# Optimization experiments

Measured on AMD Instinct MI355X. Metric: run time of the kernel, lower is better.

Reference implementation:

```python
import jax, jax.numpy as jnp
import numpy as np

# Shapes hard-coded by the original module
B, C1, C2, S, K, H, E = 128, 128, 14, 14, 3, 256, 2  # batch, chan-split, chan-split, spatial, kernel, hidden, expand


def setup_inputs() -> dict:
    key = jax.random.key(0)
    k1, k2, k3 = jax.random.split(key, 3)
    x = jax.random.normal(k1, (B, C1 * C2, S), dtype=jnp.float32)
    w0 = jax.random.normal(k2, (H, E), dtype=jnp.float32)        # weights[0]
    w1 = jax.random.normal(k3, (C1, K, H), dtype=jnp.float32)    # weights[1]
    return {"x": x, "w0": w0, "w1": w1, "shift": 1}


def reference(x, w0, w1, shift):
    # reshape to (B, C1, C2, S); original torch treats it as (B, 1792, 14, 1)
    xr = x.reshape(B, C1, C2, S)
    # unfold((3,1), padding=(1,0)): 1D im2col along the S (=14) axis
    xp = jnp.pad(xr, ((0, 0), (0, 0), (0, 0), (1, 1)))
    # patches[b, j, n, i, m] = xp[b, j, n, m + i]  -> (B, C1, C2, K, S)
    patches = jnp.stack([xp[..., k:k + S] for k in range(K)], axis=3)
    # einsum 'ljnmi,jik->lnmk' (torch had m,i swapped via permute; fold it in)
    t4 = jnp.einsum('ljnim,jik->lnmk', patches, w1)   # (B, C2, S, H)
    # einsum 'kmlj,ji->kmlji': outer product with w0 along a new expand dim
    t5 = t4[..., None] * w0                            # (B, C2, S, H, E)
    t5 = jnp.roll(t5, shift, axis=1)                   # cyclic shift over C2
    t6 = jnp.transpose(t5, (0, 2, 3, 1, 4)).reshape(B, S, H, C2 * E)
    t6 = jnp.roll(t6, shift, axis=3)                   # cyclic shift over merged (C2*E)
    t6 = t6.reshape(B, S, H, C2, E).sum(axis=4)        # (B, S, H, C2)
    return jnp.transpose(t6, (0, 2, 3, 1))             # (B, H, C2, S) = (128, 256, 14, 14)
```

## Files before the change

kernel.cpp:

```cpp
#include <hip/hip_runtime.h>
#include <hip/hip_bf16.h>
#include <math.h>

#define B_   128
#define C1_  128
#define C2_  14
#define S_   14
#define K_   3
#define H_   256
#define E_   2

#define HT   64
#define NT   4
#define MT   13
#define CH   64
#define XSTR 72
#define BSTR 200
#define CSTR 68

typedef __attribute__((ext_vector_type(8))) short bf16x8;
typedef __attribute__((ext_vector_type(4))) float f32x4;

__device__ __forceinline__ unsigned short f2bf(float f) {
    unsigned int u = __float_as_uint(f);
    return (unsigned short)((u + 0x7FFF + ((u >> 16) & 1)) >> 16);
}

__device__ __forceinline__ int decode_shift(const int* p) {
    int a = p[0];
    if (a >= -100 && a <= 100 && a != 0) return a;
    float f = __int_as_float(a);
    if (f >= -100.f && f <= 100.f && f == truncf(f) && f != 0.f) return (int)f;
    long long bits = ((long long)p[1] << 32) | (unsigned int)a;
    double d = __longlong_as_double(bits);
    if (d >= -100.0 && d <= 100.0 && d == trunc(d) && d != 0.0) return (int)d;
    return a;
}

__global__ __launch_bounds__(256, 2) void fused_kernel(const float* __restrict__ x,
                                                       const float* __restrict__ w0,
                                                       const float* __restrict__ w1,
                                                       const int* __restrict__ shift_p,
                                                       float* __restrict__ out) {
    __shared__ __align__(16) char lds[60160];
    unsigned short* xT = (unsigned short*)lds;
    unsigned short* Bt = (unsigned short*)(lds + 34560);
    float*          Cl = (float*)lds;

    const int b    = blockIdx.x >> 2;
    const int h0   = (blockIdx.x & 3) * HT;
    const int t    = threadIdx.x;
    const int wave = t >> 6;
    const int lane = t & 63;
    const int quad = lane >> 4;
    const int l15  = lane & 15;

    f32x4 acc[4][NT];
#pragma unroll
    for (int i = 0; i < 4; ++i)
#pragma unroll
        for (int j = 0; j < NT; ++j) acc[i][j] = (f32x4){0.f, 0.f, 0.f, 0.f};

    for (int hf = 0; hf < 2; ++hf) {
        if (hf) __syncthreads();
        const float* xb = x + ((size_t)b * C1_ + hf * CH) * (C2_ * S_);
        for (int idx = t; idx < CH * 196; idx += 256) {
            int c1l = idx / 196, cs = idx - c1l * 196;
            int c2 = cs / S_, s = cs - c2 * S_;
            xT[(c2 * 16 + s + 1) * XSTR + c1l] = f2bf(xb[c1l * 196 + cs]);
        }
        for (int idx = t; idx < C2_ * CH * 2; idx += 256) {
            int c2 = idx / (CH * 2), r = idx - c2 * CH * 2;
            int p = (r < CH) ? 0 : 15, c1l = (r < CH) ? r : r - CH;
            xT[(c2 * 16 + p) * XSTR + c1l] = 0;
        }
        for (int idx = t; idx < CH * K_ * HT; idx += 256) {
            int hl = idx & (HT - 1);
            int rest = idx >> 6;
            int kk = rest / CH, c1l = rest - kk * CH;
            Bt[hl * BSTR + kk * CH + c1l] =
                f2bf(w1[((size_t)(hf * CH + c1l) * K_ + kk) * H_ + h0 + hl]);
        }
        __syncthreads();

#pragma unroll
        for (int tt = 0; tt < 6; ++tt) {
            const int kk = tt >> 1;
            const int c1off = (tt & 1) * 32 + quad * 8;
            bf16x8 bf[NT];
#pragma unroll
            for (int nc = 0; nc < NT; ++nc)
                bf[nc] = *(const bf16x8*)&Bt[(nc * 16 + l15) * BSTR + tt * 32 + quad * 8];
#pragma unroll
            for (int mi = 0; mi < 4; ++mi) {
                int mt = wave + mi * 4;
                if (mt < MT) {
                    int r = mt * 16 + l15;
                    int c2 = r / 14, s = r - c2 * 14;
                    bf16x8 af = *(const bf16x8*)&xT[(c2 * 16 + s + kk) * XSTR + c1off];
#pragma unroll
                    for (int nc = 0; nc < NT; ++nc)
                        acc[mi][nc] = __builtin_amdgcn_mfma_f32_16x16x32_bf16(
                            af, bf[nc], acc[mi][nc], 0, 0, 0);
                }
            }
        }
    }

    __syncthreads();
#pragma unroll
    for (int mi = 0; mi < 4; ++mi) {
        int mt = wave + mi * 4;
        if (mt < MT) {
#pragma unroll
            for (int nc = 0; nc < NT; ++nc) {
                int hl = nc * 16 + l15;
#pragma unroll
                for (int reg = 0; reg < 4; ++reg)
                    Cl[(mt * 16 + quad * 4 + reg) * CSTR + hl] = acc[mi][nc][reg];
            }
        }
    }
    __syncthreads();

    const int shift = decode_shift(shift_p);
    for (int idx = t; idx < HT * 196; idx += 256) {
        int hl = idx / 196, nm = idx - hl * 196;
        int n = nm / S_, m = nm - n * S_;
        int h = h0 + hl;
        float v = 0.f;
#pragma unroll
        for (int e = 0; e < E_; ++e) {
            int q = (2 * n + e - shift) % (C2_ * E_); if (q < 0) q += C2_ * E_;
            int np = q >> 1, ep = q & 1;
            int c2 = (np - shift) % C2_; if (c2 < 0) c2 += C2_;
            v += w0[h * E_ + ep] * Cl[(c2 * S_ + m) * CSTR + hl];
        }
        out[((size_t)(b * H_ + h) * C2_ + n) * S_ + m] = v;
    }
}

extern "C" void kernel_launch(void* const* d_in, const int* in_sizes, int n_in,
                              void* d_out, int out_size, void* d_ws, size_t ws_size,
                              hipStream_t stream) {
    const float* x     = (const float*)d_in[0];
    const float* w0    = (const float*)d_in[1];
    const float* w1    = (const float*)d_in[2];
    const int*   shift = (const int*)(n_in > 3 ? d_in[3] : d_in[n_in - 1]);
    for (int i = 0; i < n_in; ++i) {
        int sz = in_sizes[i];
        if (sz == B_ * C1_ * C2_ * S_)      x     = (const float*)d_in[i];
        else if (sz == H_ * E_)             w0    = (const float*)d_in[i];
        else if (sz == C1_ * K_ * H_)       w1    = (const float*)d_in[i];
        else if (sz == 1)                   shift = (const int*)d_in[i];
    }
    float* out = (float*)d_out;

    fused_kernel<<<B_ * (H_ / HT), 256, 0, stream>>>(x, w0, w1, shift, out);
}
```

Measured before the change: 109.2 us.

## Pre-convert inputs to bf16 in a separate kernel and vectorize LDS staging/epilogue

Adds a conversion kernel that writes x and w1 as bf16 into workspace, so the fused kernel reads half the bytes and does not convert each element redundantly across the four h-blocks per batch. LDS fills are restructured so each thread gathers 8 channels and writes one 16-byte vector. The C tile is stored transposed (h-major) with vector stores, and the epilogue hoists the shift index math per row. The cost is an extra kernel launch plus a full extra read and write pass over x through workspace memory.

```diff
diff --git a/kernel.cpp b/kernel.cpp
--- a/kernel.cpp
+++ b/kernel.cpp
@@ -16,14 +16,16 @@
 #define CH   64
 #define XSTR 72
 #define BSTR 200
-#define CSTR 68
-
+#define CROW 212
+
+typedef unsigned short u16;
+typedef unsigned int   u32;
 typedef __attribute__((ext_vector_type(8))) short bf16x8;
 typedef __attribute__((ext_vector_type(4))) float f32x4;
 
-__device__ __forceinline__ unsigned short f2bf(float f) {
-    unsigned int u = __float_as_uint(f);
-    return (unsigned short)((u + 0x7FFF + ((u >> 16) & 1)) >> 16);
+__device__ __forceinline__ u16 f2bf(float f) {
+    u32 u = __float_as_uint(f);
+    return (u16)((u + 0x7FFF + ((u >> 16) & 1)) >> 16);
 }
 
 __device__ __forceinline__ int decode_shift(const int* p) {
@@ -37,15 +39,32 @@
     return a;
 }
 
-__global__ __launch_bounds__(256, 2) void fused_kernel(const float* __restrict__ x,
+__global__ __launch_bounds__(256) void cvt_kernel(const float* __restrict__ x,
+                                                  const float* __restrict__ w1,
+                                                  u16* __restrict__ xb,
+                                                  u16* __restrict__ w1b) {
+    const int NXq = (B_ * C1_ * C2_ * S_) / 4;
+    const int NWq = (C1_ * K_ * H_) / 4;
+    int q = blockIdx.x * 256 + threadIdx.x;
+    float4 v; u16* dst;
+    if (q < NXq)      { v = ((const float4*)x)[q];        dst = xb  + (size_t)q * 4; }
+    else { int r = q - NXq; if (r >= NWq) return;
+                       v = ((const float4*)w1)[r];        dst = w1b + (size_t)r * 4; }
+    u32 lo = (u32)f2bf(v.x) | ((u32)f2bf(v.y) << 16);
+    u32 hi = (u32)f2bf(v.z) | ((u32)f2bf(v.w) << 16);
+    *(uint2*)dst = make_uint2(lo, hi);
+}
+
+template <bool PRE>
+__global__ __launch_bounds__(256, 2) void fused_kernel(const void* __restrict__ xsrc,
                                                        const float* __restrict__ w0,
-                                                       const float* __restrict__ w1,
+                                                       const void* __restrict__ wsrc,
                                                        const int* __restrict__ shift_p,
                                                        float* __restrict__ out) {
     __shared__ __align__(16) char lds[60160];
-    unsigned short* xT = (unsigned short*)lds;
-    unsigned short* Bt = (unsigned short*)(lds + 34560);
-    float*          Cl = (float*)lds;
+    u16*   xT = (u16*)lds;
+    u16*   Bt = (u16*)(lds + 34560);
+    float* Cl = (float*)lds;
 
     const int b    = blockIdx.x >> 2;
     const int h0   = (blockIdx.x & 3) * HT;
@@ -63,23 +82,59 @@
 
     for (int hf = 0; hf < 2; ++hf) {
         if (hf) __syncthreads();
-        const float* xb = x + ((size_t)b * C1_ + hf * CH) * (C2_ * S_);
-        for (int idx = t; idx < CH * 196; idx += 256) {
-            int c1l = idx / 196, cs = idx - c1l * 196;
-            int c2 = cs / S_, s = cs - c2 * S_;
-            xT[(c2 * 16 + s + 1) * XSTR + c1l] = f2bf(xb[c1l * 196 + cs]);
-        }
-        for (int idx = t; idx < C2_ * CH * 2; idx += 256) {
-            int c2 = idx / (CH * 2), r = idx - c2 * CH * 2;
-            int p = (r < CH) ? 0 : 15, c1l = (r < CH) ? r : r - CH;
-            xT[(c2 * 16 + p) * XSTR + c1l] = 0;
-        }
-        for (int idx = t; idx < CH * K_ * HT; idx += 256) {
-            int hl = idx & (HT - 1);
-            int rest = idx >> 6;
-            int kk = rest / CH, c1l = rest - kk * CH;
-            Bt[hl * BSTR + kk * CH + c1l] =
-                f2bf(w1[((size_t)(hf * CH + c1l) * K_ + kk) * H_ + h0 + hl]);
+        {
+            const int oct = t >> 5, cs0 = t & 31;
+            const int c1b = hf * CH + oct * 8;
+#pragma unroll
+            for (int i = 0; i < 7; ++i) {
+                int cs = cs0 + 32 * i;
+                if (cs < 196) {
+                    int c2 = cs / 14, s = cs - c2 * 14;
+                    u16 v[8];
+                    if (PRE) {
+                        const u16* xbp = (const u16*)xsrc + (size_t)b * (C1_ * 196);
+#pragma unroll
+                        for (int j = 0; j < 8; ++j) v[j] = xbp[(c1b + j) * 196 + cs];
+                    } else {
+                        const float* xf = (const float*)xsrc + (size_t)b * (C1_ * 196);
+#pragma unroll
+                        for (int j = 0; j < 8; ++j) v[j] = f2bf(xf[(c1b + j) * 196 + cs]);
+                    }
+                    u32 w[4];
+#pragma unroll
+                    for (int j = 0; j < 4; ++j) w[j] = (u32)v[2 * j] | ((u32)v[2 * j + 1] << 16);
+                    *(uint4*)&xT[(c2 * 16 + s + 1) * XSTR + oct * 8] = make_uint4(w[0], w[1], w[2], w[3]);
+                }
+            }
+            if (t < 224) {
+                int c2 = t >> 4, r = t & 15;
+                int p = (r & 1) ? 15 : 0, o = r >> 1;
+                *(uint4*)&xT[(c2 * 16 + p) * XSTR + o * 8] = make_uint4(0, 0, 0, 0);
+            }
+        }
+        {
+            const int hl = t & 63, oc0 = t >> 6;
+#pragma unroll
+            for (int i = 0; i < 6; ++i) {
+                int oc = oc0 + 4 * i;
+                int kk = oc >> 3, o8 = (oc & 7) * 8;
+                u16 v[8];
+                if (PRE) {
+                    const u16* wb = (const u16*)wsrc;
+#pragma unroll
+                    for (int j = 0; j < 8; ++j)
+                        v[j] = wb[((hf * CH + o8 + j) * 3 + kk) * H_ + h0 + hl];
+                } else {
+                    const float* wf = (const float*)wsrc;
+#pragma unroll
+                    for (int j = 0; j < 8; ++j)
+                        v[j] = f2bf(wf[((hf * CH + o8 + j) * 3 + kk) * H_ + h0 + hl]);
+                }
+                u32 w[4];
+#pragma unroll
+                for (int j = 0; j < 4; ++j) w[j] = (u32)v[2 * j] | ((u32)v[2 * j + 1] << 16);
+                *(uint4*)&Bt[hl * BSTR + kk * 64 + o8] = make_uint4(w[0], w[1], w[2], w[3]);
+            }
         }
         __syncthreads();
 
@@ -115,28 +170,32 @@
 #pragma unroll
             for (int nc = 0; nc < NT; ++nc) {
                 int hl = nc * 16 + l15;
-#pragma unroll
-                for (int reg = 0; reg < 4; ++reg)
-                    Cl[(mt * 16 + quad * 4 + reg) * CSTR + hl] = acc[mi][nc][reg];
+                *(f32x4*)&Cl[hl * CROW + mt * 16 + quad * 4] = acc[mi][nc];
             }
         }
     }
     __syncthreads();
 
     const int shift = decode_shift(shift_p);
-    for (int idx = t; idx < HT * 196; idx += 256) {
-        int hl = idx / 196, nm = idx - hl * 196;
-        int n = nm / S_, m = nm - n * S_;
-        int h = h0 + hl;
-        float v = 0.f;
-#pragma unroll
-        for (int e = 0; e < E_; ++e) {
-            int q = (2 * n + e - shift) % (C2_ * E_); if (q < 0) q += C2_ * E_;
-            int np = q >> 1, ep = q & 1;
-            int c2 = (np - shift) % C2_; if (c2 < 0) c2 += C2_;
-            v += w0[h * E_ + ep] * Cl[(c2 * S_ + m) * CSTR + hl];
-        }
-        out[((size_t)(b * H_ + h) * C2_ + n) * S_ + m] = v;
+    const int hl = t >> 2, sub = t & 3;
+    const int h = h0 + hl;
+    int   c0[2]; float wv[2];
+#pragma unroll
+    for (int e = 0; e < 2; ++e) {
+        int q = (e - shift) % 28; if (q < 0) q += 28;
+        int np0 = q >> 1, ep = q & 1;
+        int c = (np0 - shift) % 14; if (c < 0) c += 14;
+        c0[e] = c;
+        wv[e] = w0[h * 2 + ep];
+    }
+    const float* Crow = &Cl[hl * CROW];
+    float* orow = out + (size_t)(b * H_ + h) * 196;
+    int m = sub, n = 0;
+    for (int i = 0; i < 49; ++i) {
+        int cA = c0[0] + n; if (cA >= 14) cA -= 14;
+        int cB = c0[1] + n; if (cB >= 14) cB -= 14;
+        orow[n * 14 + m] = wv[0] * Crow[cA * 14 + m] + wv[1] * Crow[cB * 14 + m];
+        m += 4; if (m >= 14) { m -= 14; ++n; }
     }
 }
 
@@ -156,5 +215,15 @@
     }
     float* out = (float*)d_out;
 
-    fused_kernel<<<B_ * (H_ / HT), 256, 0, stream>>>(x, w0, w1, shift, out);
-}
+    const size_t NX = (size_t)B_ * C1_ * C2_ * S_;
+    const size_t NW = (size_t)C1_ * K_ * H_;
+    if (ws_size >= (NX + NW) * sizeof(u16)) {
+        u16* xb  = (u16*)d_ws;
+        u16* w1b = xb + NX;
+        const int NQ = (int)((NX + NW) / 4);
+        cvt_kernel<<<(NQ + 255) / 256, 256, 0, stream>>>(x, w1, xb, w1b);
+        fused_kernel<true><<<B_ * (H_ / HT), 256, 0, stream>>>(xb, w0, w1b, shift, out);
+    } else {
+        fused_kernel<false><<<B_ * (H_ / HT), 256, 0, stream>>>(x, w0, w1, shift, out);
+    }
+}
```

Result: faster. 93.44 us (-14.4%).
